# Performance work log

Hardware: AMD Instinct MI355X
Metric: run time of the kernel (lower is better)

The kernel has to match this reference:

```python
import jax, jax.numpy as jnp
import numpy as np

N = 4096
IN_F = 256
OUT_F = 64
HEADS = 4
NEG_SLOPE = 0.2


def setup_inputs() -> dict:
    key = jax.random.key(0)
    k1, k2, k3, k4 = jax.random.split(key, 4)
    x = jax.random.normal(k1, (N, IN_F), dtype=jnp.float32)
    W = jax.random.normal(k2, (HEADS, IN_F, OUT_F), dtype=jnp.float32) * (1.0 / np.sqrt(IN_F))
    a = jax.random.normal(k3, (HEADS, 2 * OUT_F), dtype=jnp.float32) * (1.0 / np.sqrt(2 * OUT_F))
    adj_matrix = jax.random.randint(k4, (N, N), 0, 2, dtype=jnp.int32)
    return {"x": x, "W": W, "a": a, "adj_matrix": adj_matrix}


def reference(x, W, a, adj_matrix):
    heads, in_f, out_f = W.shape
    n = x.shape[0]
    # per-head linear transform: [H, N, F]
    xt = jnp.einsum('ni,hio->hno', x, W)
    # attention logit decomposes: a . cat(xt_i, xt_j) = src_i + dst_j
    src = jnp.einsum('hnf,hf->hn', xt, a[:, :out_f])   # [H, N]
    dst = jnp.einsum('hnf,hf->hn', xt, a[:, out_f:])   # [H, N]
    e = jax.nn.leaky_relu(src[:, :, None] + dst[:, None, :], NEG_SLOPE)  # [H, N, N]
    mask = (adj_matrix > 0)[None, :, :]
    e = jnp.where(mask, e, -jnp.inf)
    attention = jax.nn.softmax(e, axis=2)              # [H, N, N]
    # (dropout is identity in eval / p=0)
    h_prime = jnp.einsum('hij,hjf->hif', attention, xt)  # [H, N, F]
    # concat heads: [N, H*F]
    return h_prime.transpose(1, 0, 2).reshape(n, heads * out_f)
```

## Files before the change

### kernel.cpp

```cpp
#include <hip/hip_runtime.h>
#include <math.h>

#define N 4096
#define IN_F 256
#define OUT_F 64
#define HEADS 4
#define NEG 0.2f
#define JSPLIT 8
#define JLEN (N / JSPLIT)
#define NC (JLEN / 32)
#define LOG2E 1.44269504088896f

typedef float f32x4 __attribute__((ext_vector_type(4)));
typedef float f32x2 __attribute__((ext_vector_type(2)));
typedef short short8 __attribute__((ext_vector_type(8)));

#define FMA4S(A, s, V) do { (A).x = fmaf((s),(V).x,(A).x); (A).y = fmaf((s),(V).y,(A).y); \
                            (A).z = fmaf((s),(V).z,(A).z); (A).w = fmaf((s),(V).w,(A).w); } while(0)

#define MSEL(P, MS, R) (P) = __uint_as_float(__float_as_uint(P) & \
                         (unsigned)(((int)((MS) << (31 - (R)))) >> 31))

__device__ __forceinline__ unsigned short f2bf(float x) {
  unsigned int u = __float_as_uint(x);
  u += 0x7fffu + ((u >> 16) & 1u);
  return (unsigned short)(u >> 16);
}

__device__ __forceinline__ float exp2_fast(float x) {
#if __has_builtin(__builtin_amdgcn_exp2f)
  return __builtin_amdgcn_exp2f(x);
#else
  return exp2f(x);
#endif
}

__device__ __forceinline__ int pack_bf2(float p0, float p1) {
  unsigned u0 = __float_as_uint(p0) + 0x8000u;
  unsigned u1 = __float_as_uint(p1) + 0x8000u;
  return (int)__builtin_amdgcn_perm(u1, u0, 0x07060302u);
}

__global__ __launch_bounds__(256) void k_prep(const float* __restrict__ x,
                                              const float* __restrict__ W,
                                              const float* __restrict__ a,
                                              const int* __restrict__ adj,
                                              short* __restrict__ xtB,
                                              float* __restrict__ src,
                                              float* __restrict__ dst,
                                              unsigned char* __restrict__ mbB) {
  __shared__ __align__(16) float xls[32 * 68];
  __shared__ __align__(16) float wls[64 * 64];
  const int t = threadIdx.x;

  if (blockIdx.x >= 512) {
    int tid = (blockIdx.x - 512) * 256 + t;
    const int4* a4 = (const int4*)adj + (size_t)tid * 2;
    int4 v0 = a4[0];
    int4 v1 = a4[1];
    unsigned b = 0;
    b |= (v0.x > 0) ? 0x01u : 0u;
    b |= (v0.y > 0) ? 0x02u : 0u;
    b |= (v0.z > 0) ? 0x04u : 0u;
    b |= (v0.w > 0) ? 0x08u : 0u;
    b |= (v1.x > 0) ? 0x10u : 0u;
    b |= (v1.y > 0) ? 0x20u : 0u;
    b |= (v1.z > 0) ? 0x40u : 0u;
    b |= (v1.w > 0) ? 0x80u : 0u;
    mbB[tid] = (unsigned char)b;
    return;
  }

  const int h  = blockIdx.x >> 7;
  const int bx = blockIdx.x & 127;
  const int i0 = bx * 32;
  const int fg = t & 15;
  const int rg = t >> 4;

  float4 acc[2];
  acc[0] = acc[1] = make_float4(0.f, 0.f, 0.f, 0.f);

  const float4* xg = (const float4*)x;
  const float4* wg = (const float4*)W;
  float4* xls4 = (float4*)xls;
  float4* wls4 = (float4*)wls;
  const float4* xr4 = (const float4*)xls;
  const float4* wr4 = (const float4*)wls;

  for (int kt = 0; kt < 4; ++kt) {
    __syncthreads();
    #pragma unroll
    for (int s = 0; s < 2; ++s) {
      int f4i = t + 256 * s;
      int row = f4i >> 4, c4 = f4i & 15;
      xls4[row * 17 + c4] = xg[(size_t)(i0 + row) * 64 + kt * 16 + c4];
    }
    #pragma unroll
    for (int s = 0; s < 4; ++s) {
      int f4i = t + 256 * s;
      int kk = f4i >> 4, c4 = f4i & 15;
      wls4[kk * 16 + c4] = wg[(size_t)(h * 256 + kt * 64 + kk) * 16 + c4];
    }
    __syncthreads();
    #pragma unroll 4
    for (int kk = 0; kk < 64; kk += 4) {
      float4 wv0 = wr4[(kk + 0) * 16 + fg];
      float4 wv1 = wr4[(kk + 1) * 16 + fg];
      float4 wv2 = wr4[(kk + 2) * 16 + fg];
      float4 wv3 = wr4[(kk + 3) * 16 + fg];
      #pragma unroll
      for (int q = 0; q < 2; ++q) {
        float4 xv = xr4[(rg * 2 + q) * 17 + (kk >> 2)];
        FMA4S(acc[q], xv.x, wv0);
        FMA4S(acc[q], xv.y, wv1);
        FMA4S(acc[q], xv.z, wv2);
        FMA4S(acc[q], xv.w, wv3);
      }
    }
  }

  const float4* a4 = (const float4*)a;
  float4 as = a4[h * 32 + fg];
  float4 ad = a4[h * 32 + 16 + fg];
  as.x *= LOG2E; as.y *= LOG2E; as.z *= LOG2E; as.w *= LOG2E;
  ad.x *= LOG2E; ad.y *= LOG2E; ad.z *= LOG2E; ad.w *= LOG2E;
  #pragma unroll
  for (int q = 0; q < 2; ++q) {
    float s_ = acc[q].x * as.x + acc[q].y * as.y + acc[q].z * as.z + acc[q].w * as.w;
    float d_ = acc[q].x * ad.x + acc[q].y * ad.y + acc[q].z * ad.z + acc[q].w * ad.w;
    #pragma unroll
    for (int off = 1; off < 16; off <<= 1) {
      s_ += __shfl_xor(s_, off, 64);
      d_ += __shfl_xor(d_, off, 64);
    }
    if (fg == 0) {
      int r = rg * 2 + q;
      src[h * N + i0 + r] = s_;
      dst[h * N + i0 + r] = d_;
    }
  }

  __syncthreads();
  #pragma unroll
  for (int q = 0; q < 2; ++q) {
    *(float4*)&xls[(rg * 2 + q) * 68 + fg * 4] = acc[q];
  }
  __syncthreads();

  {
    const int lane = t & 63;
    const int g    = t >> 6;
    const int q    = lane >> 4;
    const int m    = lane & 15;
    short8 bv;
    #pragma unroll
    for (int r = 0; r < 8; ++r) {
      bv[r] = (short)f2bf(xls[(q * 8 + r) * 68 + g * 16 + m]);
    }
    ((short8*)xtB)[((size_t)(h * 128 + bx) * 4 + g) * 64 + lane] = bv;
  }
}

__global__ __launch_bounds__(256) void k_flash(const unsigned* __restrict__ mb,
                                               const float* __restrict__ src,
                                               const float* __restrict__ dst,
                                               const short* __restrict__ xtB,
                                               unsigned* __restrict__ accPu,
                                               float* __restrict__ lP) {
  __shared__ __align__(16) float dls[HEADS][JLEN + 4];
  const int t    = threadIdx.x;
  const int lane = t & 63;
  const int h    = t >> 6;
  const int i0   = blockIdx.x * 32;
  const int js   = blockIdx.y;
  const int q    = lane >> 4;
  const int m    = lane & 15;
  const int koff = q * 8;
  const int jbase = js * JLEN;

  #pragma unroll
  for (int s = 0; s < 2; ++s) {
    int idx = t + 256 * s;
    int hh = idx >> 7, j4 = idx & 127;
    *(float4*)&dls[hh][j4 * 4] = *(const float4*)(dst + (size_t)hh * N + jbase + j4 * 4);
  }

  float sv = (lane < 32) ? src[h * N + i0 + lane] : 0.f;
  const float s0 = __shfl(sv, m, 64);
  const float s1 = __shfl(sv, 16 + m, 64);
  __syncthreads();

  f32x4 acc0[4], acc1[4], accL0, accL1;
  #pragma unroll
  for (int g = 0; g < 4; ++g) { acc0[g] = (f32x4)(0.f); acc1[g] = (f32x4)(0.f); }
  accL0 = (f32x4)(0.f);
  accL1 = (f32x4)(0.f);

  short8 ones;
  #pragma unroll
  for (int r = 0; r < 8; ++r) ones[r] = (short)0x3F80;

  const f32x2 s02 = (f32x2)(s0);
  const f32x2 s12 = (f32x2)(s1);

  const unsigned* mrow0 = mb + (size_t)(i0 + m) * 128 + (jbase >> 5);
  const unsigned* mrow1 = mb + (size_t)(i0 + 16 + m) * 128 + (jbase >> 5);
  const short8* xbb = (const short8*)xtB + ((size_t)(h * 128 + js * NC) * 4) * 64 + lane;

#define LOADC(DM0, DM1, DB, CIDX) do {                                     \
    DM0 = mrow0[CIDX];                                                     \
    DM1 = mrow1[CIDX];                                                     \
    const short8* bb_ = xbb + (size_t)(CIDX) * 256;                        \
    DB[0] = bb_[0]; DB[1] = bb_[64]; DB[2] = bb_[128]; DB[3] = bb_[192];   \
  } while (0)

#define COMPUTE(CM0, CM1, CB, C) do {                                      \
    const float* dp_ = &dls[h][(C) * 32 + koff];                           \
    union { float4 v[2]; f32x2 h2[4]; float f[8]; } du;                    \
    du.v[0] = *(const float4*)dp_;                                         \
    du.v[1] = *(const float4*)(dp_ + 4);                                   \
    unsigned ms0 = (CM0) >> koff;                                          \
    unsigned ms1 = (CM1) >> koff;                                          \
    int av0[4], av1[4];                                                    \
    _Pragma("unroll")                                                      \
    for (int r2 = 0; r2 < 4; ++r2) {                                       \
      f32x2 d2 = du.h2[r2];                                                \
      f32x2 e0 = s02 + d2;                                                 \
      f32x2 el0 = __builtin_elementwise_max(e0, e0 * NEG);                 \
      f32x2 e1 = s12 + d2;                                                 \
      f32x2 el1 = __builtin_elementwise_max(e1, e1 * NEG);                 \
      float p0a = exp2_fast(el0.x), p0b = exp2_fast(el0.y);                \
      float p1a = exp2_fast(el1.x), p1b = exp2_fast(el1.y);                \
      MSEL(p0a, ms0, 2 * r2);  MSEL(p0b, ms0, 2 * r2 + 1);                 \
      MSEL(p1a, ms1, 2 * r2);  MSEL(p1b, ms1, 2 * r2 + 1);                 \
      av0[r2] = pack_bf2(p0a, p0b);                                        \
      av1[r2] = pack_bf2(p1a, p1b);                                        \
    }                                                                      \
    short8 af0 = __builtin_bit_cast(short8, *(int4*)av0);                  \
    short8 af1 = __builtin_bit_cast(short8, *(int4*)av1);                  \
    acc0[0] = __builtin_amdgcn_mfma_f32_16x16x32_bf16(af0, CB[0], acc0[0], 0, 0, 0); \
    acc0[1] = __builtin_amdgcn_mfma_f32_16x16x32_bf16(af0, CB[1], acc0[1], 0, 0, 0); \
    acc0[2] = __builtin_amdgcn_mfma_f32_16x16x32_bf16(af0, CB[2], acc0[2], 0, 0, 0); \
    acc0[3] = __builtin_amdgcn_mfma_f32_16x16x32_bf16(af0, CB[3], acc0[3], 0, 0, 0); \
    accL0   = __builtin_amdgcn_mfma_f32_16x16x32_bf16(af0, ones,  accL0,   0, 0, 0); \
    acc1[0] = __builtin_amdgcn_mfma_f32_16x16x32_bf16(af1, CB[0], acc1[0], 0, 0, 0); \
    acc1[1] = __builtin_amdgcn_mfma_f32_16x16x32_bf16(af1, CB[1], acc1[1], 0, 0, 0); \
    acc1[2] = __builtin_amdgcn_mfma_f32_16x16x32_bf16(af1, CB[2], acc1[2], 0, 0, 0); \
    acc1[3] = __builtin_amdgcn_mfma_f32_16x16x32_bf16(af1, CB[3], acc1[3], 0, 0, 0); \
    accL1   = __builtin_amdgcn_mfma_f32_16x16x32_bf16(af1, ones,  accL1,   0, 0, 0); \
  } while (0)

  unsigned cM0, cM1, nM0, nM1;
  short8 cB[4], nB[4];
  LOADC(cM0, cM1, cB, 0);

  for (int c = 0; c < NC; ++c) {
    const int cn = (c + 1 < NC) ? c + 1 : c;
    LOADC(nM0, nM1, nB, cn);

    COMPUTE(cM0, cM1, cB, c);

    cM0 = nM0; cM1 = nM1;
    #pragma unroll
    for (int z = 0; z < 4; ++z) cB[z] = nB[z];
  }
#undef LOADC
#undef COMPUTE

  float* lp = lP + (size_t)js * (HEADS * N);
  if (m == 0) {
    #pragma unroll
    for (int reg = 0; reg < 4; ++reg) {
      lp[h * N + i0 + q * 4 + reg] = accL0[reg];
      lp[h * N + i0 + 16 + q * 4 + reg] = accL1[reg];
    }
  }

  unsigned* ap = accPu + (size_t)js * ((size_t)HEADS * N * 32);
  #pragma unroll
  for (int reg = 0; reg < 4; ++reg) {
    int row0 = i0 + q * 4 + reg;
    int row1 = row0 + 16;
    ap[((size_t)h * N + row0) * 32 + m]      = (unsigned)pack_bf2(acc0[0][reg], acc0[1][reg]);
    ap[((size_t)h * N + row0) * 32 + 16 + m] = (unsigned)pack_bf2(acc0[2][reg], acc0[3][reg]);
    ap[((size_t)h * N + row1) * 32 + m]      = (unsigned)pack_bf2(acc1[0][reg], acc1[1][reg]);
    ap[((size_t)h * N + row1) * 32 + 16 + m] = (unsigned)pack_bf2(acc1[2][reg], acc1[3][reg]);
  }
}

__global__ __launch_bounds__(256) void k_div(const unsigned* __restrict__ accPu,
                                             const float* __restrict__ lP,
                                             float* __restrict__ out) {
  int v = blockIdx.x * 256 + threadIdx.x;
  int col4 = v & 63;
  int i    = v >> 6;
  int h    = col4 >> 4;
  int fl   = (col4 & 15) * 4;
  int g    = fl >> 4;
  int m0   = fl & 15;
  size_t base = ((size_t)h * N + i) * 32 + (size_t)((g >> 1) * 16 + m0);
  const int hi = g & 1;
  float4 s = make_float4(0.f, 0.f, 0.f, 0.f);
  float ls = 0.f;
  #pragma unroll
  for (int js = 0; js < JSPLIT; ++js) {
    const uint4 u = *(const uint4*)(accPu + (size_t)js * ((size_t)HEADS * N * 32) + base);
    s.x += __uint_as_float(hi ? (u.x & 0xffff0000u) : (u.x << 16));
    s.y += __uint_as_float(hi ? (u.y & 0xffff0000u) : (u.y << 16));
    s.z += __uint_as_float(hi ? (u.z & 0xffff0000u) : (u.z << 16));
    s.w += __uint_as_float(hi ? (u.w & 0xffff0000u) : (u.w << 16));
    ls += lP[(size_t)js * (HEADS * N) + h * N + i];
  }
  float il = 1.f / ls;
  ((float4*)out)[v] = make_float4(s.x * il, s.y * il, s.z * il, s.w * il);
}

extern "C" void kernel_launch(void* const* d_in, const int* in_sizes, int n_in,
                              void* d_out, int out_size, void* d_ws, size_t ws_size,
                              hipStream_t stream) {
  const float* x   = (const float*)d_in[0];
  const float* W   = (const float*)d_in[1];
  const float* a   = (const float*)d_in[2];
  const int*   adj = (const int*)d_in[3];
  float* out = (float*)d_out;

  float* ws    = (float*)d_ws;
  short* xtB   = (short*)ws;
  float* src   = ws + 524288;
  float* dst   = src + HEADS * N;
  unsigned* accPu = (unsigned*)(dst + HEADS * N);
  float* lP    = (float*)(accPu + (size_t)JSPLIT * HEADS * N * 32);
  unsigned* mb = (unsigned*)(lP + JSPLIT * HEADS * N);

  k_prep<<<dim3(512 + N * N / 8 / 256), 256, 0, stream>>>(x, W, a, adj, xtB, src, dst,
                                                          (unsigned char*)mb);
  k_flash<<<dim3(N / 32, JSPLIT), 256, 0, stream>>>(mb, src, dst, xtB, accPu, lP);
  k_div<<<dim3((N * OUT_F) / 256), 256, 0, stream>>>(accPu, lP, out);
}
```

Before: 140.2 us.

## Fuse split-J reduction into flash kernel via last-block atomic counter

Removes the separate k_div launch. Each k_flash block bumps a per-row-tile counter after writing its partial results, and the last of the JSPLIT blocks for that tile reduces the partials and normalizes them into the output. This saves a kernel launch and its gap, and lets the reduction overlap with other flash blocks. In exchange it adds threadfences and atomics, and the final reduction runs on only the last block for each tile. The counters are zeroed in k_prep.

```diff
diff --git a/kernel.cpp b/kernel.cpp
--- a/kernel.cpp
+++ b/kernel.cpp
@@ -48,12 +48,14 @@
                                               short* __restrict__ xtB,
                                               float* __restrict__ src,
                                               float* __restrict__ dst,
-                                              unsigned char* __restrict__ mbB) {
+                                              unsigned char* __restrict__ mbB,
+                                              int* __restrict__ cnt) {
   __shared__ __align__(16) float xls[32 * 68];
   __shared__ __align__(16) float wls[64 * 64];
   const int t = threadIdx.x;
 
   if (blockIdx.x >= 512) {
+    if (blockIdx.x == 512 && t < 128) cnt[t] = 0;
     int tid = (blockIdx.x - 512) * 256 + t;
     const int4* a4 = (const int4*)adj + (size_t)tid * 2;
     int4 v0 = a4[0];
@@ -166,8 +168,11 @@
                                                const float* __restrict__ dst,
                                                const short* __restrict__ xtB,
                                                unsigned* __restrict__ accPu,
-                                               float* __restrict__ lP) {
+                                               float* __restrict__ lP,
+                                               int* __restrict__ cnt,
+                                               float* __restrict__ out) {
   __shared__ __align__(16) float dls[HEADS][JLEN + 4];
+  __shared__ int is_last;
   const int t    = threadIdx.x;
   const int lane = t & 63;
   const int h    = t >> 6;
@@ -286,33 +291,38 @@
     ap[((size_t)h * N + row1) * 32 + m]      = (unsigned)pack_bf2(acc1[0][reg], acc1[1][reg]);
     ap[((size_t)h * N + row1) * 32 + 16 + m] = (unsigned)pack_bf2(acc1[2][reg], acc1[3][reg]);
   }
-}
-
-__global__ __launch_bounds__(256) void k_div(const unsigned* __restrict__ accPu,
-                                             const float* __restrict__ lP,
-                                             float* __restrict__ out) {
-  int v = blockIdx.x * 256 + threadIdx.x;
-  int col4 = v & 63;
-  int i    = v >> 6;
-  int h    = col4 >> 4;
-  int fl   = (col4 & 15) * 4;
-  int g    = fl >> 4;
-  int m0   = fl & 15;
-  size_t base = ((size_t)h * N + i) * 32 + (size_t)((g >> 1) * 16 + m0);
-  const int hi = g & 1;
-  float4 s = make_float4(0.f, 0.f, 0.f, 0.f);
-  float ls = 0.f;
-  #pragma unroll
-  for (int js = 0; js < JSPLIT; ++js) {
-    const uint4 u = *(const uint4*)(accPu + (size_t)js * ((size_t)HEADS * N * 32) + base);
-    s.x += __uint_as_float(hi ? (u.x & 0xffff0000u) : (u.x << 16));
-    s.y += __uint_as_float(hi ? (u.y & 0xffff0000u) : (u.y << 16));
-    s.z += __uint_as_float(hi ? (u.z & 0xffff0000u) : (u.z << 16));
-    s.w += __uint_as_float(hi ? (u.w & 0xffff0000u) : (u.w << 16));
-    ls += lP[(size_t)js * (HEADS * N) + h * N + i];
-  }
-  float il = 1.f / ls;
-  ((float4*)out)[v] = make_float4(s.x * il, s.y * il, s.z * il, s.w * il);
+
+  __threadfence();
+  if (t == 0) is_last = (atomicAdd(&cnt[blockIdx.x], 1) == JSPLIT - 1);
+  __syncthreads();
+  if (!is_last) return;
+  __threadfence();
+
+  #pragma unroll
+  for (int w8 = 0; w8 < 8; ++w8) {
+    int w = t + w8 * 256;
+    int col4 = w & 63;
+    int i    = i0 + (w >> 6);
+    int hh   = col4 >> 4;
+    int fl   = (col4 & 15) * 4;
+    int g    = fl >> 4;
+    int m0   = fl & 15;
+    size_t base = ((size_t)hh * N + i) * 32 + (size_t)((g >> 1) * 16 + m0);
+    const int hi = g & 1;
+    float4 s = make_float4(0.f, 0.f, 0.f, 0.f);
+    float ls = 0.f;
+    #pragma unroll
+    for (int j2 = 0; j2 < JSPLIT; ++j2) {
+      const uint4 u = *(const uint4*)(accPu + (size_t)j2 * ((size_t)HEADS * N * 32) + base);
+      s.x += __uint_as_float(hi ? (u.x & 0xffff0000u) : (u.x << 16));
+      s.y += __uint_as_float(hi ? (u.y & 0xffff0000u) : (u.y << 16));
+      s.z += __uint_as_float(hi ? (u.z & 0xffff0000u) : (u.z << 16));
+      s.w += __uint_as_float(hi ? (u.w & 0xffff0000u) : (u.w << 16));
+      ls += lP[(size_t)j2 * (HEADS * N) + hh * N + i];
+    }
+    float il = 1.f / ls;
+    ((float4*)out)[(size_t)i * 64 + col4] = make_float4(s.x * il, s.y * il, s.z * il, s.w * il);
+  }
 }
 
 extern "C" void kernel_launch(void* const* d_in, const int* in_sizes, int n_in,
@@ -331,9 +341,9 @@
   unsigned* accPu = (unsigned*)(dst + HEADS * N);
   float* lP    = (float*)(accPu + (size_t)JSPLIT * HEADS * N * 32);
   unsigned* mb = (unsigned*)(lP + JSPLIT * HEADS * N);
+  int* cnt     = (int*)(mb + N * 128);
 
   k_prep<<<dim3(512 + N * N / 8 / 256), 256, 0, stream>>>(x, W, a, adj, xtB, src, dst,
-                                                          (unsigned char*)mb);
-  k_flash<<<dim3(N / 32, JSPLIT), 256, 0, stream>>>(mb, src, dst, xtB, accPu, lP);
-  k_div<<<dim3((N * OUT_F) / 256), 256, 0, stream>>>(accPu, lP, out);
-}
+                                                          (unsigned char*)mb, cnt);
+  k_flash<<<dim3(N / 32, JSPLIT), 256, 0, stream>>>(mb, src, dst, xtB, accPu, lP, cnt, out);
+}
```

New measurement: 266.3 us. +90.0%, slower.
